# Optimization experiments

Measured on AMD Instinct MI355X. Metric: run time of the kernel, lower is better.

Reference implementation:

```python
import jax, jax.numpy as jnp
import numpy as np

V = 100001; H = 64; E = 768; S = 200; B = 256; NB = 2; NH = 2; HD = H // NH

def ln(x, g, b, eps):
    m = x.mean(-1, keepdims=True)
    v = ((x - m) ** 2).mean(-1, keepdims=True)
    return (x - m) / jnp.sqrt(v + eps) * g + b

def setup_inputs():
    key = jax.random.key(0)
    ks = jax.random.split(key, 32)
    f = lambda i, shape: (0.02 * jax.random.normal(ks[i], shape)).astype(jnp.float32)
    inp = {}
    inp['targetSeq'] = jax.random.randint(ks[0], (B, S), 0, V)
    inp['pos'] = jax.random.randint(ks[1], (B, S), 0, V)
    inp['neg'] = jax.random.randint(ks[2], (B, S), 0, V)
    inp['review_emb'] = f(3, (V, E))
    inp['meta_emb'] = f(4, (V, E))
    inp['item_emb'] = f(5, (V, H))
    inp['pos_emb_table'] = f(6, (S, H))
    inp['featW'] = f(7, (E, H))
    inp['featb'] = jnp.zeros((H,), jnp.float32)
    inp['revln_g'] = jnp.ones((H,), jnp.float32)
    inp['revln_b'] = jnp.zeros((H,), jnp.float32)
    for j, n in enumerate(['Wq', 'Wk', 'Wv', 'Wpq', 'Wpk', 'Wfq', 'Wfk', 'Wo', 'W1', 'W2']):
        inp[n] = f(8 + j, (NB, H, H))
    for n in ['bq', 'bk', 'bv', 'bpq', 'bpk', 'bfq', 'bfk', 'bo', 'b1', 'b2']:
        inp[n] = jnp.zeros((NB, H), jnp.float32)
    inp['attn_ln_g'] = jnp.ones((NB, H), jnp.float32)
    inp['attn_ln_b'] = jnp.zeros((NB, H), jnp.float32)
    inp['fwd_ln_g'] = jnp.ones((NB, H), jnp.float32)
    inp['fwd_ln_b'] = jnp.zeros((NB, H), jnp.float32)
    inp['lastln_g'] = jnp.ones((H,), jnp.float32)
    inp['lastln_b'] = jnp.zeros((H,), jnp.float32)
    return inp

def reference(targetSeq, pos, neg, review_emb, meta_emb, item_emb, pos_emb_table, featW, featb, revln_g, revln_b, Wq, Wk, Wv, Wpq, Wpk, Wfq, Wfk, Wo, W1, W2, bq, bk, bv, bpq, bpk, bfq, bfk, bo, b1, b2, attn_ln_g, attn_ln_b, fwd_ln_g, fwd_ln_b, lastln_g, lastln_b):
    Bv, Sv = targetSeq.shape
    keep = (targetSeq != 0).astype(jnp.float32)[..., None]  # [B,S,1] timeline mask
    # feat_emb: fused review+meta features -> linear -> LayerNorm (eps=1e-5)
    feat = ln((review_emb[targetSeq] + meta_emb[targetSeq]) @ featW + featb, revln_g, revln_b, 1e-5)
    pe = jnp.broadcast_to(pos_emb_table[None, :Sv], (Bv, Sv, H))
    q = item_emb[targetSeq] * keep
    causal = jnp.where(jnp.tril(jnp.ones((Sv, Sv), bool)), 0.0, -jnp.inf).astype(jnp.float32)
    scale = 1.0 / jnp.sqrt(jnp.float32(HD))
    heads = lambda x: x.reshape(Bv, Sv, NH, HD)
    for i in range(NB):
        Qn = ln(q, attn_ln_g[i], attn_ln_b[i], 1e-8)
        qh = heads(Qn @ Wq[i] + bq[i])
        kh = heads(q @ Wk[i] + bk[i])
        vh = heads(q @ Wv[i] + bv[i])
        pq = heads(pe @ Wpq[i] + bpq[i]); pk = heads(pe @ Wpk[i] + bpk[i])
        fq = heads(feat @ Wfq[i] + bfq[i]); fk = heads(feat @ Wfk[i] + bfk[i])
        # decoupled (DIF) attention: item + position + feature score terms
        scores = (jnp.einsum('bqhd,bkhd->bhqk', qh, kh)
                  + jnp.einsum('bqhd,bkhd->bhqk', pq, pk)
                  + jnp.einsum('bqhd,bkhd->bhqk', fq, fk)) * scale + causal
        probs = jax.nn.softmax(scores, axis=-1)
        ctx = jnp.einsum('bhqk,bkhd->bqhd', probs, vh).reshape(Bv, Sv, H)
        q = ctx @ Wo[i] + bo[i] + Qn  # residual with pre-LN branch
        q = ln(q, fwd_ln_g[i], fwd_ln_b[i], 1e-8)
        q = jax.nn.relu(q @ W1[i] + b1[i]) @ W2[i] + b2[i] + q  # 1x1-conv FFN + residual
        q = q * keep
    log_feats = ln(q, lastln_g, lastln_b, 1e-8)
    pos_logits = jnp.sum(log_feats * item_emb[pos], axis=-1)
    neg_logits = jnp.sum(log_feats * item_emb[neg], axis=-1)
    return (pos_logits, neg_logits)
```

## Files before the change

kernel.cpp:

```cpp
#include <hip/hip_runtime.h>

#define DEV __device__ __forceinline__

typedef __attribute__((ext_vector_type(4))) float f32x4;
typedef __attribute__((ext_vector_type(8))) __bf16 bf16x8;

static constexpr int Bc = 256;
static constexpr int Sc = 200;
static constexpr int Hc = 64;
static constexpr int Ec = 768;
static constexpr int HDc = 32;
static constexpr int NROWS = Bc * Sc;

DEV __bf16 f2bf(float f) {
    unsigned u = __builtin_bit_cast(unsigned, f);
    unsigned r = (u + 0x7fffu + ((u >> 16) & 1u)) >> 16;
    unsigned short s = (unsigned short)r;
    return __builtin_bit_cast(__bf16, s);
}

DEV bf16x8 load_frag8(const float* __restrict__ p) {
    f32x4 a = *(const f32x4*)p;
    f32x4 b = *(const f32x4*)(p + 4);
    bf16x8 r;
    r[0] = f2bf(a[0]); r[1] = f2bf(a[1]); r[2] = f2bf(a[2]); r[3] = f2bf(a[3]);
    r[4] = f2bf(b[0]); r[5] = f2bf(b[1]); r[6] = f2bf(b[2]); r[7] = f2bf(b[3]);
    return r;
}

DEV bf16x8 load_wfrag(const float* __restrict__ W, int k0, int n) {
    bf16x8 r;
#pragma unroll
    for (int j = 0; j < 8; j++) r[j] = f2bf(W[(k0 + j) * Hc + n]);
    return r;
}

__global__ __launch_bounds__(256) void feat_kernel(
    const int* __restrict__ tseq, const float* __restrict__ rev,
    const float* __restrict__ meta, const float* __restrict__ featW,
    const float* __restrict__ featb, const float* __restrict__ g,
    const float* __restrict__ bb, float* __restrict__ out)
{
    int lane = threadIdx.x & 63, wv = threadIdx.x >> 6;
    int ln = lane & 15, quad = lane >> 4;
    int m0 = blockIdx.x * 64 + wv * 16;
    long t = tseq[m0 + ln];
    const float* rp = rev + t * Ec + quad * 8;
    const float* mp = meta + t * Ec + quad * 8;

    f32x4 acc[4];
#pragma unroll
    for (int nt = 0; nt < 4; nt++) acc[nt] = (f32x4){0.f, 0.f, 0.f, 0.f};

    for (int ks = 0; ks < Ec / 32; ks++) {
        f32x4 ra = *(const f32x4*)(rp + ks * 32);
        f32x4 rb = *(const f32x4*)(rp + ks * 32 + 4);
        f32x4 ma = *(const f32x4*)(mp + ks * 32);
        f32x4 mb = *(const f32x4*)(mp + ks * 32 + 4);
        bf16x8 a;
        a[0] = f2bf(ra[0] + ma[0]); a[1] = f2bf(ra[1] + ma[1]);
        a[2] = f2bf(ra[2] + ma[2]); a[3] = f2bf(ra[3] + ma[3]);
        a[4] = f2bf(rb[0] + mb[0]); a[5] = f2bf(rb[1] + mb[1]);
        a[6] = f2bf(rb[2] + mb[2]); a[7] = f2bf(rb[3] + mb[3]);
#pragma unroll
        for (int nt = 0; nt < 4; nt++) {
            bf16x8 bf = load_wfrag(featW, ks * 32 + quad * 8, nt * 16 + ln);
            acc[nt] = __builtin_amdgcn_mfma_f32_16x16x32_bf16(a, bf, acc[nt], 0, 0, 0);
        }
    }
#pragma unroll
    for (int reg = 0; reg < 4; reg++) {
        float vals[4]; float s = 0.f, s2 = 0.f;
#pragma unroll
        for (int nt = 0; nt < 4; nt++) {
            float v = acc[nt][reg] + featb[nt * 16 + ln];
            vals[nt] = v; s += v; s2 += v * v;
        }
#pragma unroll
        for (int m = 1; m <= 8; m <<= 1) { s += __shfl_xor(s, m, 64); s2 += __shfl_xor(s2, m, 64); }
        float mean = s * (1.f / 64.f);
        float var = s2 * (1.f / 64.f) - mean * mean;
        float inv = rsqrtf(var + 1e-5f);
        int r = m0 + quad * 4 + reg;
#pragma unroll
        for (int nt = 0; nt < 4; nt++) {
            int c = nt * 16 + ln;
            out[r * Hc + c] = (vals[nt] - mean) * inv * g[c] + bb[c];
        }
    }
}

__global__ __launch_bounds__(256) void qinit_kernel(
    const int* __restrict__ tseq, const float* __restrict__ item, float* __restrict__ q)
{
    int gid = blockIdx.x * 256 + threadIdx.x;
    int r = gid >> 4, c4 = (gid & 15) * 4;
    long t = tseq[r];
    f32x4 v = *(const f32x4*)(item + t * Hc + c4);
    float k = (t != 0) ? 1.f : 0.f;
    v *= k;
    *(f32x4*)(q + (long)r * Hc + c4) = v;
}

__global__ __launch_bounds__(256) void proj_kernel(
    const float* __restrict__ X, int Nrows,
    const float* __restrict__ W0, const float* __restrict__ b0, float* __restrict__ Y0,
    const float* __restrict__ W1, const float* __restrict__ b1, float* __restrict__ Y1,
    const float* __restrict__ res, const int* __restrict__ keep, int doRelu)
{
    int lane = threadIdx.x & 63, wv = threadIdx.x >> 6;
    int ln = lane & 15, quad = lane >> 4;
    int m0 = blockIdx.x * 64 + wv * 16;
    int arow = m0 + ln; if (arow > Nrows - 1) arow = Nrows - 1;
    bf16x8 a0 = load_frag8(X + (long)arow * Hc + quad * 8);
    bf16x8 a1 = load_frag8(X + (long)arow * Hc + 32 + quad * 8);

    int nsets = (W1 != nullptr) ? 2 : 1;
    for (int si = 0; si < nsets; si++) {
        const float* W = si ? W1 : W0;
        const float* bias = si ? b1 : b0;
        float* Y = si ? Y1 : Y0;
#pragma unroll
        for (int nt = 0; nt < 4; nt++) {
            int col = nt * 16 + ln;
            bf16x8 w0 = load_wfrag(W, quad * 8, col);
            bf16x8 w1 = load_wfrag(W, 32 + quad * 8, col);
            f32x4 acc = (f32x4){0.f, 0.f, 0.f, 0.f};
            acc = __builtin_amdgcn_mfma_f32_16x16x32_bf16(a0, w0, acc, 0, 0, 0);
            acc = __builtin_amdgcn_mfma_f32_16x16x32_bf16(a1, w1, acc, 0, 0, 0);
            float bv = bias[col];
#pragma unroll
            for (int reg = 0; reg < 4; reg++) {
                int r = m0 + quad * 4 + reg;
                if (r < Nrows) {
                    float v = acc[reg] + bv;
                    if (doRelu) v = fmaxf(v, 0.f);
                    if (res) v += res[(long)r * Hc + col];
                    if (keep) v *= (keep[r] != 0) ? 1.f : 0.f;
                    Y[(long)r * Hc + col] = v;
                }
            }
        }
    }
}

__global__ __launch_bounds__(256) void ln_rows(
    const float* __restrict__ X, const float* __restrict__ g,
    const float* __restrict__ b, float* __restrict__ Y, float eps)
{
    int row = blockIdx.x * 4 + (threadIdx.x >> 6);
    int lane = threadIdx.x & 63;
    float v = X[(long)row * Hc + lane];
    float s = v, s2 = v * v;
#pragma unroll
    for (int m = 1; m <= 32; m <<= 1) { s += __shfl_xor(s, m, 64); s2 += __shfl_xor(s2, m, 64); }
    float mean = s * (1.f / 64.f);
    float var = s2 * (1.f / 64.f) - mean * mean;
    Y[(long)row * Hc + lane] = (v - mean) * rsqrtf(var + eps) * g[lane] + b[lane];
}

__global__ __launch_bounds__(256) void attn_kernel(
    const float* __restrict__ qp, const float* __restrict__ kp, const float* __restrict__ vp,
    const float* __restrict__ pqp, const float* __restrict__ pkp,
    const float* __restrict__ fqp, const float* __restrict__ fkp,
    float* __restrict__ ctx)
{
    __shared__ float Sm[16 * 208];
    __shared__ __bf16 Vt[32 * 224];

    int bb = blockIdx.x >> 1, h = blockIdx.x & 1;
    int tid = threadIdx.x;
    int lane = tid & 63, wv = tid >> 6;
    int ln = lane & 15, quad = lane >> 4;
    const int hc = h * HDc;
    const long base = (long)bb * Sc;
    const float scale = 0.17677669529663687f;
    __bf16* P = (__bf16*)Sm;

    for (int idx = tid; idx < Sc * HDc; idx += 256) {
        int k = idx >> 5, n = idx & 31;
        Vt[n * 224 + k] = f2bf(vp[(base + k) * Hc + hc + n]);
    }
    for (int idx = tid; idx < HDc * 24; idx += 256) {
        int n = idx / 24, k = 200 + idx % 24;
        Vt[n * 224 + k] = __builtin_bit_cast(__bf16, (unsigned short)0);
    }

    for (int t = 0; t < 13; t++) {
        __syncthreads();
        int arow = t * 16 + ln; if (arow > Sc - 1) arow = Sc - 1;
        bf16x8 aq0 = load_frag8(qp + (base + arow) * Hc + hc + quad * 8);
        bf16x8 aq1 = load_frag8(pqp + (long)arow * Hc + hc + quad * 8);
        bf16x8 aq2 = load_frag8(fqp + (base + arow) * Hc + hc + quad * 8);
        for (int nt = wv; nt <= t; nt += 4) {
            int key = nt * 16 + ln; if (key > Sc - 1) key = Sc - 1;
            f32x4 acc = (f32x4){0.f, 0.f, 0.f, 0.f};
            bf16x8 b0 = load_frag8(kp + (base + key) * Hc + hc + quad * 8);
            acc = __builtin_amdgcn_mfma_f32_16x16x32_bf16(aq0, b0, acc, 0, 0, 0);
            bf16x8 b1 = load_frag8(pkp + (long)key * Hc + hc + quad * 8);
            acc = __builtin_amdgcn_mfma_f32_16x16x32_bf16(aq1, b1, acc, 0, 0, 0);
            bf16x8 b2 = load_frag8(fkp + (base + key) * Hc + hc + quad * 8);
            acc = __builtin_amdgcn_mfma_f32_16x16x32_bf16(aq2, b2, acc, 0, 0, 0);
#pragma unroll
            for (int reg = 0; reg < 4; reg++)
                Sm[(quad * 4 + reg) * 208 + nt * 16 + ln] = acc[reg] * scale;
        }
        __syncthreads();
        for (int ri = 0; ri < 4; ri++) {
            int r = wv * 4 + ri;
            int qrow = t * 16 + r;
            float sv[4]; float mx = -1e30f;
#pragma unroll
            for (int j = 0; j < 4; j++) {
                int k = lane + 64 * j;
                sv[j] = (k <= qrow && k < 208) ? Sm[r * 208 + k] : -1e30f;
                mx = fmaxf(mx, sv[j]);
            }
#pragma unroll
            for (int m = 1; m <= 32; m <<= 1) mx = fmaxf(mx, __shfl_xor(mx, m, 64));
            float sum = 0.f; float pv[4];
#pragma unroll
            for (int j = 0; j < 4; j++) {
                float e = (sv[j] > -1e29f) ? __expf(sv[j] - mx) : 0.f;
                pv[j] = e; sum += e;
            }
#pragma unroll
            for (int m = 1; m <= 32; m <<= 1) sum += __shfl_xor(sum, m, 64);
            float inv = 1.f / sum;
#pragma unroll
            for (int j = 0; j < 4; j++) {
                int k = lane + 64 * j;
                if (k < 224) P[r * 416 + k] = f2bf(pv[j] * inv);
            }
        }
        __syncthreads();
        if (wv < 2) {
            int ksteps = (t + 2) >> 1;
            f32x4 acc = (f32x4){0.f, 0.f, 0.f, 0.f};
            const char* Pb = (const char*)Sm;
            for (int ks = 0; ks < ksteps; ks++) {
                bf16x8 pa = *(const bf16x8*)(Pb + ln * 832 + ks * 64 + quad * 16);
                bf16x8 vb = *(const bf16x8*)(&Vt[(wv * 16 + ln) * 224 + ks * 32 + quad * 8]);
                acc = __builtin_amdgcn_mfma_f32_16x16x32_bf16(pa, vb, acc, 0, 0, 0);
            }
#pragma unroll
            for (int reg = 0; reg < 4; reg++) {
                int r = t * 16 + quad * 4 + reg;
                if (r < Sc) ctx[(base + r) * Hc + hc + wv * 16 + ln] = acc[reg];
            }
        }
    }
}

__global__ __launch_bounds__(256) void logits_kernel(
    const float* __restrict__ lf, const int* __restrict__ pos, const int* __restrict__ neg,
    const float* __restrict__ item, float* __restrict__ out)
{
    int row = blockIdx.x * 4 + (threadIdx.x >> 6);
    int lane = threadIdx.x & 63;
    float v = lf[(long)row * Hc + lane];
    long p = pos[row], n = neg[row];
    float dp = v * item[p * Hc + lane];
    float dn = v * item[n * Hc + lane];
#pragma unroll
    for (int m = 1; m <= 32; m <<= 1) { dp += __shfl_xor(dp, m, 64); dn += __shfl_xor(dn, m, 64); }
    if (lane == 0) { out[row] = dp; out[NROWS + row] = dn; }
}

extern "C" void kernel_launch(void* const* d_in, const int* in_sizes, int n_in,
                              void* d_out, int out_size, void* d_ws, size_t ws_size,
                              hipStream_t stream)
{
    const int* tseq = (const int*)d_in[0];
    const int* pos  = (const int*)d_in[1];
    const int* neg  = (const int*)d_in[2];
    const float* rev   = (const float*)d_in[3];
    const float* meta  = (const float*)d_in[4];
    const float* item  = (const float*)d_in[5];
    const float* pe    = (const float*)d_in[6];
    const float* featW = (const float*)d_in[7];
    const float* featb = (const float*)d_in[8];
    const float* rg    = (const float*)d_in[9];
    const float* rb    = (const float*)d_in[10];
    const float* Wq = (const float*)d_in[11]; const float* Wk = (const float*)d_in[12];
    const float* Wv = (const float*)d_in[13]; const float* Wpq = (const float*)d_in[14];
    const float* Wpk = (const float*)d_in[15]; const float* Wfq = (const float*)d_in[16];
    const float* Wfk = (const float*)d_in[17]; const float* Wo = (const float*)d_in[18];
    const float* W1 = (const float*)d_in[19]; const float* W2 = (const float*)d_in[20];
    const float* bq = (const float*)d_in[21]; const float* bk = (const float*)d_in[22];
    const float* bv = (const float*)d_in[23]; const float* bpq = (const float*)d_in[24];
    const float* bpk = (const float*)d_in[25]; const float* bfq = (const float*)d_in[26];
    const float* bfk = (const float*)d_in[27]; const float* bo = (const float*)d_in[28];
    const float* b1 = (const float*)d_in[29]; const float* b2 = (const float*)d_in[30];
    const float* ag = (const float*)d_in[31]; const float* ab = (const float*)d_in[32];
    const float* fg = (const float*)d_in[33]; const float* fb = (const float*)d_in[34];
    const float* lg = (const float*)d_in[35]; const float* lb = (const float*)d_in[36];
    float* out = (float*)d_out;

    float* ws = (float*)d_ws;
    const size_t F = (size_t)NROWS * Hc;
    float* feat = ws;
    float* q    = ws + 1 * F;
    float* Qn   = ws + 2 * F;
    float* qp   = ws + 3 * F;
    float* kp   = ws + 4 * F;
    float* vp   = ws + 5 * F;
    float* fqp  = ws + 6 * F;
    float* fkp  = ws + 7 * F;
    float* pqp  = ws + 8 * F;
    float* pkp  = pqp + (size_t)Sc * Hc;

    const int PB = NROWS / 64;
    const int LB = NROWS / 4;

    feat_kernel<<<PB, 256, 0, stream>>>(tseq, rev, meta, featW, featb, rg, rb, feat);
    qinit_kernel<<<NROWS * Hc / 4 / 256, 256, 0, stream>>>(tseq, item, q);

    for (int i = 0; i < 2; i++) {
        const float* Wq_i = Wq + i * Hc * Hc;  const float* bq_i = bq + i * Hc;
        const float* Wk_i = Wk + i * Hc * Hc;  const float* bk_i = bk + i * Hc;
        const float* Wv_i = Wv + i * Hc * Hc;  const float* bv_i = bv + i * Hc;
        const float* Wpq_i = Wpq + i * Hc * Hc; const float* bpq_i = bpq + i * Hc;
        const float* Wpk_i = Wpk + i * Hc * Hc; const float* bpk_i = bpk + i * Hc;
        const float* Wfq_i = Wfq + i * Hc * Hc; const float* bfq_i = bfq + i * Hc;
        const float* Wfk_i = Wfk + i * Hc * Hc; const float* bfk_i = bfk + i * Hc;
        const float* Wo_i = Wo + i * Hc * Hc;  const float* bo_i = bo + i * Hc;
        const float* W1_i = W1 + i * Hc * Hc;  const float* b1_i = b1 + i * Hc;
        const float* W2_i = W2 + i * Hc * Hc;  const float* b2_i = b2 + i * Hc;

        ln_rows<<<LB, 256, 0, stream>>>(q, ag + i * Hc, ab + i * Hc, Qn, 1e-8f);
        proj_kernel<<<PB, 256, 0, stream>>>(Qn, NROWS, Wq_i, bq_i, qp,
                                            nullptr, nullptr, nullptr, nullptr, nullptr, 0);
        proj_kernel<<<PB, 256, 0, stream>>>(q, NROWS, Wk_i, bk_i, kp,
                                            Wv_i, bv_i, vp, nullptr, nullptr, 0);
        proj_kernel<<<PB, 256, 0, stream>>>(feat, NROWS, Wfq_i, bfq_i, fqp,
                                            Wfk_i, bfk_i, fkp, nullptr, nullptr, 0);
        proj_kernel<<<(Sc + 63) / 64, 256, 0, stream>>>(pe, Sc, Wpq_i, bpq_i, pqp,
                                            Wpk_i, bpk_i, pkp, nullptr, nullptr, 0);
        attn_kernel<<<Bc * 2, 256, 0, stream>>>(qp, kp, vp, pqp, pkp, fqp, fkp, qp);
        proj_kernel<<<PB, 256, 0, stream>>>(qp, NROWS, Wo_i, bo_i, q,
                                            nullptr, nullptr, nullptr, Qn, nullptr, 0);
        ln_rows<<<LB, 256, 0, stream>>>(q, fg + i * Hc, fb + i * Hc, q, 1e-8f);
        proj_kernel<<<PB, 256, 0, stream>>>(q, NROWS, W1_i, b1_i, kp,
                                            nullptr, nullptr, nullptr, nullptr, nullptr, 1);
        proj_kernel<<<PB, 256, 0, stream>>>(kp, NROWS, W2_i, b2_i, q,
                                            nullptr, nullptr, nullptr, q, tseq, 0);
    }
    ln_rows<<<LB, 256, 0, stream>>>(q, lg, lb, q, 1e-8f);
    logits_kernel<<<LB, 256, 0, stream>>>(q, pos, neg, item, out);
}
```

Baseline: 1.037 ms.

## Store activations in bf16, pre-transpose weights, fuse projections/LN/FFN into few kernels

```diff
diff --git a/kernel.cpp b/kernel.cpp
--- a/kernel.cpp
+++ b/kernel.cpp
@@ -14,12 +14,17 @@
 
 DEV __bf16 f2bf(float f) {
     unsigned u = __builtin_bit_cast(unsigned, f);
-    unsigned r = (u + 0x7fffu + ((u >> 16) & 1u)) >> 16;
-    unsigned short s = (unsigned short)r;
+    unsigned short s = (unsigned short)((u + 0x7fffu + ((u >> 16) & 1u)) >> 16);
     return __builtin_bit_cast(__bf16, s);
 }
-
-DEV bf16x8 load_frag8(const float* __restrict__ p) {
+DEV float bf2f(__bf16 h) {
+    unsigned short s = __builtin_bit_cast(unsigned short, h);
+    unsigned u = ((unsigned)s) << 16;
+    return __builtin_bit_cast(float, u);
+}
+DEV bf16x8 ld8(const __bf16* p) { return *(const bf16x8*)p; }
+
+DEV bf16x8 cvt8(const float* __restrict__ p) {
     f32x4 a = *(const f32x4*)p;
     f32x4 b = *(const f32x4*)(p + 4);
     bf16x8 r;
@@ -28,18 +33,52 @@
     return r;
 }
 
-DEV bf16x8 load_wfrag(const float* __restrict__ W, int k0, int n) {
-    bf16x8 r;
-#pragma unroll
-    for (int j = 0; j < 8; j++) r[j] = f2bf(W[(k0 + j) * Hc + n]);
-    return r;
+DEV void gemm64(bf16x8 A0, bf16x8 A1, const __bf16* __restrict__ W,
+                const float* __restrict__ bias, __bf16* __restrict__ Y,
+                int m0, int ln, int quad, int maxrow)
+{
+#pragma unroll
+    for (int nt = 0; nt < 4; nt++) {
+        int col = nt * 16 + ln;
+        bf16x8 w0 = ld8(W + col * 64 + quad * 8);
+        bf16x8 w1 = ld8(W + col * 64 + 32 + quad * 8);
+        f32x4 acc = (f32x4){0.f, 0.f, 0.f, 0.f};
+        acc = __builtin_amdgcn_mfma_f32_16x16x32_bf16(A0, w0, acc, 0, 0, 0);
+        acc = __builtin_amdgcn_mfma_f32_16x16x32_bf16(A1, w1, acc, 0, 0, 0);
+        float bv = bias[col];
+#pragma unroll
+        for (int reg = 0; reg < 4; reg++) {
+            int r = m0 + quad * 4 + reg;
+            if (r < maxrow) Y[(long)r * 64 + col] = f2bf(acc[reg] + bv);
+        }
+    }
+}
+
+__global__ __launch_bounds__(256) void wconv_kernel(
+    const float* __restrict__ featW,
+    const float* __restrict__ Wq, const float* __restrict__ Wk, const float* __restrict__ Wv,
+    const float* __restrict__ Wpq, const float* __restrict__ Wpk,
+    const float* __restrict__ Wfq, const float* __restrict__ Wfk,
+    const float* __restrict__ Wo, const float* __restrict__ W1, const float* __restrict__ W2,
+    __bf16* __restrict__ featWt, __bf16* __restrict__ Wt)
+{
+    int gid = blockIdx.x * 256 + threadIdx.x;
+    if (gid < Ec * Hc) {
+        int k = gid >> 6, n = gid & 63;
+        featWt[n * Ec + k] = f2bf(featW[gid]);
+        return;
+    }
+    int e2 = gid - Ec * Hc;
+    int mat = e2 >> 13, r = e2 & 8191, l = r >> 12, e = r & 4095, k = e >> 6, n = e & 63;
+    const float* Ws[10] = {Wq, Wk, Wv, Wpq, Wpk, Wfq, Wfk, Wo, W1, W2};
+    Wt[mat * 8192 + l * 4096 + n * 64 + k] = f2bf(Ws[mat][l * 4096 + e]);
 }
 
 __global__ __launch_bounds__(256) void feat_kernel(
     const int* __restrict__ tseq, const float* __restrict__ rev,
-    const float* __restrict__ meta, const float* __restrict__ featW,
+    const float* __restrict__ meta, const __bf16* __restrict__ featWt,
     const float* __restrict__ featb, const float* __restrict__ g,
-    const float* __restrict__ bb, float* __restrict__ out)
+    const float* __restrict__ bb, __bf16* __restrict__ out)
 {
     int lane = threadIdx.x & 63, wv = threadIdx.x >> 6;
     int ln = lane & 15, quad = lane >> 4;
@@ -64,7 +103,7 @@
         a[6] = f2bf(rb[2] + mb[2]); a[7] = f2bf(rb[3] + mb[3]);
 #pragma unroll
         for (int nt = 0; nt < 4; nt++) {
-            bf16x8 bf = load_wfrag(featW, ks * 32 + quad * 8, nt * 16 + ln);
+            bf16x8 bf = ld8(featWt + (nt * 16 + ln) * Ec + ks * 32 + quad * 8);
             acc[nt] = __builtin_amdgcn_mfma_f32_16x16x32_bf16(a, bf, acc[nt], 0, 0, 0);
         }
     }
@@ -85,85 +124,93 @@
 #pragma unroll
         for (int nt = 0; nt < 4; nt++) {
             int c = nt * 16 + ln;
-            out[r * Hc + c] = (vals[nt] - mean) * inv * g[c] + bb[c];
+            out[(long)r * Hc + c] = f2bf((vals[nt] - mean) * inv * g[c] + bb[c]);
         }
     }
 }
 
 __global__ __launch_bounds__(256) void qinit_kernel(
-    const int* __restrict__ tseq, const float* __restrict__ item, float* __restrict__ q)
+    const int* __restrict__ tseq, const float* __restrict__ item, __bf16* __restrict__ q)
 {
     int gid = blockIdx.x * 256 + threadIdx.x;
-    int r = gid >> 4, c4 = (gid & 15) * 4;
+    int r = gid >> 3, c = (gid & 7) * 8;
     long t = tseq[r];
-    f32x4 v = *(const f32x4*)(item + t * Hc + c4);
+    f32x4 v0 = *(const f32x4*)(item + t * Hc + c);
+    f32x4 v1 = *(const f32x4*)(item + t * Hc + c + 4);
     float k = (t != 0) ? 1.f : 0.f;
-    v *= k;
-    *(f32x4*)(q + (long)r * Hc + c4) = v;
-}
-
-__global__ __launch_bounds__(256) void proj_kernel(
-    const float* __restrict__ X, int Nrows,
-    const float* __restrict__ W0, const float* __restrict__ b0, float* __restrict__ Y0,
-    const float* __restrict__ W1, const float* __restrict__ b1, float* __restrict__ Y1,
-    const float* __restrict__ res, const int* __restrict__ keep, int doRelu)
+    bf16x8 o;
+    o[0] = f2bf(v0[0] * k); o[1] = f2bf(v0[1] * k); o[2] = f2bf(v0[2] * k); o[3] = f2bf(v0[3] * k);
+    o[4] = f2bf(v1[0] * k); o[5] = f2bf(v1[1] * k); o[6] = f2bf(v1[2] * k); o[7] = f2bf(v1[3] * k);
+    *(bf16x8*)(q + (long)r * Hc + c) = o;
+}
+
+__global__ __launch_bounds__(256) void pe_kernel(
+    const float* __restrict__ pe, const __bf16* __restrict__ Wt,
+    const float* __restrict__ bpq, const float* __restrict__ bpk,
+    __bf16* __restrict__ pqp, __bf16* __restrict__ pkp)
+{
+    int l = blockIdx.x >> 2, rb = blockIdx.x & 3;
+    int lane = threadIdx.x & 63, wv = threadIdx.x >> 6;
+    int ln = lane & 15, quad = lane >> 4;
+    int m0 = rb * 64 + wv * 16;
+    int arow = m0 + ln; if (arow > Sc - 1) arow = Sc - 1;
+    bf16x8 a0 = cvt8(pe + arow * Hc + quad * 8);
+    bf16x8 a1 = cvt8(pe + arow * Hc + 32 + quad * 8);
+    gemm64(a0, a1, Wt + 3 * 8192 + l * 4096, bpq + l * 64, pqp + l * Sc * Hc, m0, ln, quad, Sc);
+    gemm64(a0, a1, Wt + 4 * 8192 + l * 4096, bpk + l * 64, pkp + l * Sc * Hc, m0, ln, quad, Sc);
+}
+
+__global__ __launch_bounds__(256) void qkvf_kernel(
+    const __bf16* __restrict__ q, const __bf16* __restrict__ feat,
+    const __bf16* __restrict__ Wt, int layer,
+    const float* __restrict__ bq, const float* __restrict__ bk, const float* __restrict__ bv,
+    const float* __restrict__ bfq, const float* __restrict__ bfk,
+    const float* __restrict__ ag, const float* __restrict__ ab,
+    __bf16* __restrict__ Qn, __bf16* __restrict__ qp, __bf16* __restrict__ kp,
+    __bf16* __restrict__ vp, __bf16* __restrict__ fqp, __bf16* __restrict__ fkp)
 {
     int lane = threadIdx.x & 63, wv = threadIdx.x >> 6;
     int ln = lane & 15, quad = lane >> 4;
     int m0 = blockIdx.x * 64 + wv * 16;
-    int arow = m0 + ln; if (arow > Nrows - 1) arow = Nrows - 1;
-    bf16x8 a0 = load_frag8(X + (long)arow * Hc + quad * 8);
-    bf16x8 a1 = load_frag8(X + (long)arow * Hc + 32 + quad * 8);
-
-    int nsets = (W1 != nullptr) ? 2 : 1;
-    for (int si = 0; si < nsets; si++) {
-        const float* W = si ? W1 : W0;
-        const float* bias = si ? b1 : b0;
-        float* Y = si ? Y1 : Y0;
-#pragma unroll
-        for (int nt = 0; nt < 4; nt++) {
-            int col = nt * 16 + ln;
-            bf16x8 w0 = load_wfrag(W, quad * 8, col);
-            bf16x8 w1 = load_wfrag(W, 32 + quad * 8, col);
-            f32x4 acc = (f32x4){0.f, 0.f, 0.f, 0.f};
-            acc = __builtin_amdgcn_mfma_f32_16x16x32_bf16(a0, w0, acc, 0, 0, 0);
-            acc = __builtin_amdgcn_mfma_f32_16x16x32_bf16(a1, w1, acc, 0, 0, 0);
-            float bv = bias[col];
-#pragma unroll
-            for (int reg = 0; reg < 4; reg++) {
-                int r = m0 + quad * 4 + reg;
-                if (r < Nrows) {
-                    float v = acc[reg] + bv;
-                    if (doRelu) v = fmaxf(v, 0.f);
-                    if (res) v += res[(long)r * Hc + col];
-                    if (keep) v *= (keep[r] != 0) ? 1.f : 0.f;
-                    Y[(long)r * Hc + col] = v;
-                }
-            }
-        }
-    }
-}
-
-__global__ __launch_bounds__(256) void ln_rows(
-    const float* __restrict__ X, const float* __restrict__ g,
-    const float* __restrict__ b, float* __restrict__ Y, float eps)
-{
-    int row = blockIdx.x * 4 + (threadIdx.x >> 6);
-    int lane = threadIdx.x & 63;
-    float v = X[(long)row * Hc + lane];
-    float s = v, s2 = v * v;
-#pragma unroll
-    for (int m = 1; m <= 32; m <<= 1) { s += __shfl_xor(s, m, 64); s2 += __shfl_xor(s2, m, 64); }
+    long row = m0 + ln;
+    bf16x8 aq0 = ld8(q + row * 64 + quad * 8);
+    bf16x8 aq1 = ld8(q + row * 64 + 32 + quad * 8);
+    bf16x8 af0 = ld8(feat + row * 64 + quad * 8);
+    bf16x8 af1 = ld8(feat + row * 64 + 32 + quad * 8);
+
+    float s = 0.f, s2 = 0.f;
+#pragma unroll
+    for (int j = 0; j < 8; j++) {
+        float v = bf2f(aq0[j]); s += v; s2 += v * v;
+        v = bf2f(aq1[j]); s += v; s2 += v * v;
+    }
+    s += __shfl_xor(s, 16, 64); s += __shfl_xor(s, 32, 64);
+    s2 += __shfl_xor(s2, 16, 64); s2 += __shfl_xor(s2, 32, 64);
     float mean = s * (1.f / 64.f);
-    float var = s2 * (1.f / 64.f) - mean * mean;
-    Y[(long)row * Hc + lane] = (v - mean) * rsqrtf(var + eps) * g[lane] + b[lane];
+    float inv = rsqrtf(s2 * (1.f / 64.f) - mean * mean + 1e-8f);
+    const float* agl = ag + layer * 64; const float* abl = ab + layer * 64;
+    bf16x8 nq0, nq1;
+#pragma unroll
+    for (int j = 0; j < 8; j++) {
+        int k0 = quad * 8 + j, k1 = 32 + quad * 8 + j;
+        nq0[j] = f2bf((bf2f(aq0[j]) - mean) * inv * agl[k0] + abl[k0]);
+        nq1[j] = f2bf((bf2f(aq1[j]) - mean) * inv * agl[k1] + abl[k1]);
+    }
+    *(bf16x8*)(Qn + row * 64 + quad * 8) = nq0;
+    *(bf16x8*)(Qn + row * 64 + 32 + quad * 8) = nq1;
+
+    gemm64(nq0, nq1, Wt + 0 * 8192 + layer * 4096, bq + layer * 64, qp, m0, ln, quad, NROWS);
+    gemm64(aq0, aq1, Wt + 1 * 8192 + layer * 4096, bk + layer * 64, kp, m0, ln, quad, NROWS);
+    gemm64(aq0, aq1, Wt + 2 * 8192 + layer * 4096, bv + layer * 64, vp, m0, ln, quad, NROWS);
+    gemm64(af0, af1, Wt + 5 * 8192 + layer * 4096, bfq + layer * 64, fqp, m0, ln, quad, NROWS);
+    gemm64(af0, af1, Wt + 6 * 8192 + layer * 4096, bfk + layer * 64, fkp, m0, ln, quad, NROWS);
 }
 
 __global__ __launch_bounds__(256) void attn_kernel(
-    const float* __restrict__ qp, const float* __restrict__ kp, const float* __restrict__ vp,
-    const float* __restrict__ pqp, const float* __restrict__ pkp,
-    const float* __restrict__ fqp, const float* __restrict__ fkp,
-    float* __restrict__ ctx)
+    const __bf16* __restrict__ qp, const __bf16* __restrict__ kp, const __bf16* __restrict__ vp,
+    const __bf16* __restrict__ pqp, const __bf16* __restrict__ pkp,
+    const __bf16* __restrict__ fqp, const __bf16* __restrict__ fkp,
+    __bf16* __restrict__ ctx)
 {
     __shared__ float Sm[16 * 208];
     __shared__ __bf16 Vt[32 * 224];
@@ -179,7 +226,7 @@
 
     for (int idx = tid; idx < Sc * HDc; idx += 256) {
         int k = idx >> 5, n = idx & 31;
-        Vt[n * 224 + k] = f2bf(vp[(base + k) * Hc + hc + n]);
+        Vt[n * 224 + k] = vp[(base + k) * Hc + hc + n];
     }
     for (int idx = tid; idx < HDc * 24; idx += 256) {
         int n = idx / 24, k = 200 + idx % 24;
@@ -189,18 +236,15 @@
     for (int t = 0; t < 13; t++) {
         __syncthreads();
         int arow = t * 16 + ln; if (arow > Sc - 1) arow = Sc - 1;
-        bf16x8 aq0 = load_frag8(qp + (base + arow) * Hc + hc + quad * 8);
-        bf16x8 aq1 = load_frag8(pqp + (long)arow * Hc + hc + quad * 8);
-        bf16x8 aq2 = load_frag8(fqp + (base + arow) * Hc + hc + quad * 8);
+        bf16x8 aq0 = ld8(qp + (base + arow) * Hc + hc + quad * 8);
+        bf16x8 aq1 = ld8(pqp + (long)arow * Hc + hc + quad * 8);
+        bf16x8 aq2 = ld8(fqp + (base + arow) * Hc + hc + quad * 8);
         for (int nt = wv; nt <= t; nt += 4) {
             int key = nt * 16 + ln; if (key > Sc - 1) key = Sc - 1;
             f32x4 acc = (f32x4){0.f, 0.f, 0.f, 0.f};
-            bf16x8 b0 = load_frag8(kp + (base + key) * Hc + hc + quad * 8);
-            acc = __builtin_amdgcn_mfma_f32_16x16x32_bf16(aq0, b0, acc, 0, 0, 0);
-            bf16x8 b1 = load_frag8(pkp + (long)key * Hc + hc + quad * 8);
-            acc = __builtin_amdgcn_mfma_f32_16x16x32_bf16(aq1, b1, acc, 0, 0, 0);
-            bf16x8 b2 = load_frag8(fkp + (base + key) * Hc + hc + quad * 8);
-            acc = __builtin_amdgcn_mfma_f32_16x16x32_bf16(aq2, b2, acc, 0, 0, 0);
+            acc = __builtin_amdgcn_mfma_f32_16x16x32_bf16(aq0, ld8(kp + (base + key) * Hc + hc + quad * 8), acc, 0, 0, 0);
+            acc = __builtin_amdgcn_mfma_f32_16x16x32_bf16(aq1, ld8(pkp + (long)key * Hc + hc + quad * 8), acc, 0, 0, 0);
+            acc = __builtin_amdgcn_mfma_f32_16x16x32_bf16(aq2, ld8(fkp + (base + key) * Hc + hc + quad * 8), acc, 0, 0, 0);
 #pragma unroll
             for (int reg = 0; reg < 4; reg++)
                 Sm[(quad * 4 + reg) * 208 + nt * 16 + ln] = acc[reg] * scale;
@@ -246,22 +290,119 @@
 #pragma unroll
             for (int reg = 0; reg < 4; reg++) {
                 int r = t * 16 + quad * 4 + reg;
-                if (r < Sc) ctx[(base + r) * Hc + hc + wv * 16 + ln] = acc[reg];
+                if (r < Sc) ctx[(base + r) * Hc + hc + wv * 16 + ln] = f2bf(acc[reg]);
             }
         }
     }
 }
 
+__global__ __launch_bounds__(256) void ffn_kernel(
+    const __bf16* __restrict__ ctx, const __bf16* __restrict__ Qn,
+    const __bf16* __restrict__ WtO, const __bf16* __restrict__ Wt1, const __bf16* __restrict__ Wt2,
+    const float* __restrict__ bo, const float* __restrict__ b1, const float* __restrict__ b2,
+    const float* __restrict__ fg, const float* __restrict__ fb,
+    const int* __restrict__ tseq, __bf16* __restrict__ qout)
+{
+    __shared__ __bf16 T1[4][16 * 64];
+    __shared__ __bf16 T2[4][16 * 64];
+    int lane = threadIdx.x & 63, wv = threadIdx.x >> 6;
+    int ln = lane & 15, quad = lane >> 4;
+    int m0 = blockIdx.x * 64 + wv * 16;
+
+    bf16x8 ac0 = ld8(ctx + (long)(m0 + ln) * 64 + quad * 8);
+    bf16x8 ac1 = ld8(ctx + (long)(m0 + ln) * 64 + 32 + quad * 8);
+
+    float tv[16];
+#pragma unroll
+    for (int nt = 0; nt < 4; nt++) {
+        int col = nt * 16 + ln;
+        bf16x8 w0 = ld8(WtO + col * 64 + quad * 8);
+        bf16x8 w1 = ld8(WtO + col * 64 + 32 + quad * 8);
+        f32x4 acc = (f32x4){0.f, 0.f, 0.f, 0.f};
+        acc = __builtin_amdgcn_mfma_f32_16x16x32_bf16(ac0, w0, acc, 0, 0, 0);
+        acc = __builtin_amdgcn_mfma_f32_16x16x32_bf16(ac1, w1, acc, 0, 0, 0);
+        float bov = bo[col];
+#pragma unroll
+        for (int reg = 0; reg < 4; reg++)
+            tv[nt * 4 + reg] = acc[reg] + bov + bf2f(Qn[(long)(m0 + quad * 4 + reg) * 64 + col]);
+    }
+    float s[4] = {0, 0, 0, 0}, s2[4] = {0, 0, 0, 0};
+#pragma unroll
+    for (int reg = 0; reg < 4; reg++)
+#pragma unroll
+        for (int nt = 0; nt < 4; nt++) { float v = tv[nt * 4 + reg]; s[reg] += v; s2[reg] += v * v; }
+#pragma unroll
+    for (int m = 1; m <= 8; m <<= 1)
+#pragma unroll
+        for (int reg = 0; reg < 4; reg++) { s[reg] += __shfl_xor(s[reg], m, 64); s2[reg] += __shfl_xor(s2[reg], m, 64); }
+    float uv[16];
+#pragma unroll
+    for (int reg = 0; reg < 4; reg++) {
+        float mean = s[reg] * (1.f / 64.f);
+        float inv = rsqrtf(s2[reg] * (1.f / 64.f) - mean * mean + 1e-8f);
+#pragma unroll
+        for (int nt = 0; nt < 4; nt++) {
+            int col = nt * 16 + ln;
+            float u = (tv[nt * 4 + reg] - mean) * inv * fg[col] + fb[col];
+            uv[nt * 4 + reg] = u;
+            T1[wv][(quad * 4 + reg) * 64 + col] = f2bf(u);
+        }
+    }
+    __syncthreads();
+    bf16x8 au0 = ld8(&T1[wv][ln * 64 + quad * 8]);
+    bf16x8 au1 = ld8(&T1[wv][ln * 64 + 32 + quad * 8]);
+#pragma unroll
+    for (int nt = 0; nt < 4; nt++) {
+        int col = nt * 16 + ln;
+        bf16x8 w0 = ld8(Wt1 + col * 64 + quad * 8);
+        bf16x8 w1 = ld8(Wt1 + col * 64 + 32 + quad * 8);
+        f32x4 acc = (f32x4){0.f, 0.f, 0.f, 0.f};
+        acc = __builtin_amdgcn_mfma_f32_16x16x32_bf16(au0, w0, acc, 0, 0, 0);
+        acc = __builtin_amdgcn_mfma_f32_16x16x32_bf16(au1, w1, acc, 0, 0, 0);
+        float b1v = b1[col];
+#pragma unroll
+        for (int reg = 0; reg < 4; reg++)
+            T2[wv][(quad * 4 + reg) * 64 + col] = f2bf(fmaxf(acc[reg] + b1v, 0.f));
+    }
+    __syncthreads();
+    bf16x8 ah0 = ld8(&T2[wv][ln * 64 + quad * 8]);
+    bf16x8 ah1 = ld8(&T2[wv][ln * 64 + 32 + quad * 8]);
+#pragma unroll
+    for (int nt = 0; nt < 4; nt++) {
+        int col = nt * 16 + ln;
+        bf16x8 w0 = ld8(Wt2 + col * 64 + quad * 8);
+        bf16x8 w1 = ld8(Wt2 + col * 64 + 32 + quad * 8);
+        f32x4 acc = (f32x4){0.f, 0.f, 0.f, 0.f};
+        acc = __builtin_amdgcn_mfma_f32_16x16x32_bf16(ah0, w0, acc, 0, 0, 0);
+        acc = __builtin_amdgcn_mfma_f32_16x16x32_bf16(ah1, w1, acc, 0, 0, 0);
+        float b2v = b2[col];
+#pragma unroll
+        for (int reg = 0; reg < 4; reg++) {
+            int r = m0 + quad * 4 + reg;
+            float v = acc[reg] + b2v + uv[nt * 4 + reg];
+            v *= (tseq[r] != 0) ? 1.f : 0.f;
+            qout[(long)r * 64 + col] = f2bf(v);
+        }
+    }
+}
+
 __global__ __launch_bounds__(256) void logits_kernel(
-    const float* __restrict__ lf, const int* __restrict__ pos, const int* __restrict__ neg,
-    const float* __restrict__ item, float* __restrict__ out)
+    const __bf16* __restrict__ q, const int* __restrict__ pos, const int* __restrict__ neg,
+    const float* __restrict__ item, const float* __restrict__ lg, const float* __restrict__ lb,
+    float* __restrict__ out)
 {
     int row = blockIdx.x * 4 + (threadIdx.x >> 6);
     int lane = threadIdx.x & 63;
-    float v = lf[(long)row * Hc + lane];
+    float v = bf2f(q[(long)row * Hc + lane]);
+    float s = v, s2 = v * v;
+#pragma unroll
+    for (int m = 1; m <= 32; m <<= 1) { s += __shfl_xor(s, m, 64); s2 += __shfl_xor(s2, m, 64); }
+    float mean = s * (1.f / 64.f);
+    float inv = rsqrtf(s2 * (1.f / 64.f) - mean * mean + 1e-8f);
+    float lf = (v - mean) * inv * lg[lane] + lb[lane];
     long p = pos[row], n = neg[row];
-    float dp = v * item[p * Hc + lane];
-    float dn = v * item[n * Hc + lane];
+    float dp = lf * item[p * Hc + lane];
+    float dn = lf * item[n * Hc + lane];
 #pragma unroll
     for (int m = 1; m <= 32; m <<= 1) { dp += __shfl_xor(dp, m, 64); dn += __shfl_xor(dn, m, 64); }
     if (lane == 0) { out[row] = dp; out[NROWS + row] = dn; }
@@ -297,55 +438,43 @@
     const float* lg = (const float*)d_in[35]; const float* lb = (const float*)d_in[36];
     float* out = (float*)d_out;
 
-    float* ws = (float*)d_ws;
+    __bf16* wsb = (__bf16*)d_ws;
     const size_t F = (size_t)NROWS * Hc;
-    float* feat = ws;
-    float* q    = ws + 1 * F;
-    float* Qn   = ws + 2 * F;
-    float* qp   = ws + 3 * F;
-    float* kp   = ws + 4 * F;
-    float* vp   = ws + 5 * F;
-    float* fqp  = ws + 6 * F;
-    float* fkp  = ws + 7 * F;
-    float* pqp  = ws + 8 * F;
-    float* pkp  = pqp + (size_t)Sc * Hc;
+    __bf16* feat = wsb;
+    __bf16* q    = wsb + 1 * F;
+    __bf16* Qn   = wsb + 2 * F;
+    __bf16* qp   = wsb + 3 * F;
+    __bf16* kp   = wsb + 4 * F;
+    __bf16* vp   = wsb + 5 * F;
+    __bf16* fqp  = wsb + 6 * F;
+    __bf16* fkp  = wsb + 7 * F;
+    __bf16* pqp  = wsb + 8 * F;
+    __bf16* pkp  = pqp + 2 * Sc * Hc;
+    __bf16* featWt = pkp + 2 * Sc * Hc;
+    __bf16* Wt     = featWt + Ec * Hc;
 
     const int PB = NROWS / 64;
     const int LB = NROWS / 4;
 
-    feat_kernel<<<PB, 256, 0, stream>>>(tseq, rev, meta, featW, featb, rg, rb, feat);
-    qinit_kernel<<<NROWS * Hc / 4 / 256, 256, 0, stream>>>(tseq, item, q);
+    wconv_kernel<<<512, 256, 0, stream>>>(featW, Wq, Wk, Wv, Wpq, Wpk, Wfq, Wfk, Wo, W1, W2,
+                                          featWt, Wt);
+    qinit_kernel<<<NROWS * Hc / 8 / 256, 256, 0, stream>>>(tseq, item, q);
+    feat_kernel<<<PB, 256, 0, stream>>>(tseq, rev, meta, featWt, featb, rg, rb, feat);
+    pe_kernel<<<8, 256, 0, stream>>>(pe, Wt, bpq, bpk, pqp, pkp);
 
     for (int i = 0; i < 2; i++) {
-        const float* Wq_i = Wq + i * Hc * Hc;  const float* bq_i = bq + i * Hc;
-        const float* Wk_i = Wk + i * Hc * Hc;  const float* bk_i = bk + i * Hc;
-        const float* Wv_i = Wv + i * Hc * Hc;  const float* bv_i = bv + i * Hc;
-        const float* Wpq_i = Wpq + i * Hc * Hc; const float* bpq_i = bpq + i * Hc;
-        const float* Wpk_i = Wpk + i * Hc * Hc; const float* bpk_i = bpk + i * Hc;
-        const float* Wfq_i = Wfq + i * Hc * Hc; const float* bfq_i = bfq + i * Hc;
-        const float* Wfk_i = Wfk + i * Hc * Hc; const float* bfk_i = bfk + i * Hc;
-        const float* Wo_i = Wo + i * Hc * Hc;  const float* bo_i = bo + i * Hc;
-        const float* W1_i = W1 + i * Hc * Hc;  const float* b1_i = b1 + i * Hc;
-        const float* W2_i = W2 + i * Hc * Hc;  const float* b2_i = b2 + i * Hc;
-
-        ln_rows<<<LB, 256, 0, stream>>>(q, ag + i * Hc, ab + i * Hc, Qn, 1e-8f);
-        proj_kernel<<<PB, 256, 0, stream>>>(Qn, NROWS, Wq_i, bq_i, qp,
-                                            nullptr, nullptr, nullptr, nullptr, nullptr, 0);
-        proj_kernel<<<PB, 256, 0, stream>>>(q, NROWS, Wk_i, bk_i, kp,
-                                            Wv_i, bv_i, vp, nullptr, nullptr, 0);
-        proj_kernel<<<PB, 256, 0, stream>>>(feat, NROWS, Wfq_i, bfq_i, fqp,
-                                            Wfk_i, bfk_i, fkp, nullptr, nullptr, 0);
-        proj_kernel<<<(Sc + 63) / 64, 256, 0, stream>>>(pe, Sc, Wpq_i, bpq_i, pqp,
-                                            Wpk_i, bpk_i, pkp, nullptr, nullptr, 0);
-        attn_kernel<<<Bc * 2, 256, 0, stream>>>(qp, kp, vp, pqp, pkp, fqp, fkp, qp);
-        proj_kernel<<<PB, 256, 0, stream>>>(qp, NROWS, Wo_i, bo_i, q,
-                                            nullptr, nullptr, nullptr, Qn, nullptr, 0);
-        ln_rows<<<LB, 256, 0, stream>>>(q, fg + i * Hc, fb + i * Hc, q, 1e-8f);
-        proj_kernel<<<PB, 256, 0, stream>>>(q, NROWS, W1_i, b1_i, kp,
-                                            nullptr, nullptr, nullptr, nullptr, nullptr, 1);
-        proj_kernel<<<PB, 256, 0, stream>>>(kp, NROWS, W2_i, b2_i, q,
-                                            nullptr, nullptr, nullptr, q, tseq, 0);
-    }
-    ln_rows<<<LB, 256, 0, stream>>>(q, lg, lb, q, 1e-8f);
-    logits_kernel<<<LB, 256, 0, stream>>>(q, pos, neg, item, out);
-}
+        qkvf_kernel<<<PB, 256, 0, stream>>>(q, feat, Wt, i,
+                                            bq, bk, bv, bfq, bfk, ag, ab,
+                                            Qn, qp, kp, vp, fqp, fkp);
+        attn_kernel<<<Bc * 2, 256, 0, stream>>>(qp, kp, vp,
+                                                pqp + i * Sc * Hc, pkp + i * Sc * Hc,
+                                                fqp, fkp, qp);
+        ffn_kernel<<<PB, 256, 0, stream>>>(qp, Qn,
+                                           Wt + 7 * 8192 + i * 4096,
+                                           Wt + 8 * 8192 + i * 4096,
+                                           Wt + 9 * 8192 + i * 4096,
+                                           bo + i * 64, b1 + i * 64, b2 + i * 64,
+                                           fg + i * 64, fb + i * 64, tseq, q);
+    }
+    logits_kernel<<<LB, 256, 0, stream>>>(q, pos, neg, item, lg, lb, out);
+}
```

Measured after the change: 883.2 us. 14.8% less time.
